# Kernel optimization log

Measured on AMD Instinct MI355X. Metric: run time of the kernel, lower is better.

The kernel has to match this reference:

```python
import jax, jax.numpy as jnp
import numpy as np

N = 8192
E = 262144
D_IN = 256
D_OUT = 256

def setup_inputs() -> dict:
    key = jax.random.key(0)
    k1, k2, k3, k4 = jax.random.split(key, 4)
    x = jax.random.normal(k1, (N, D_IN), dtype=jnp.float32)
    edge_index = jax.random.randint(k2, (2, E), 0, N, dtype=jnp.int64)
    W = jax.random.normal(k3, (D_OUT, D_IN), dtype=jnp.float32) * (1.0 / np.sqrt(D_IN))
    b = jax.random.normal(k4, (D_OUT,), dtype=jnp.float32) * 0.01
    return {"x": x, "edge_index": edge_index, "W": W, "b": b}

def reference(x, edge_index, W, b):
    num_nodes = x.shape[0]
    # dense adjacency: adj[src, dst] = 1.0 (duplicates collapse to 1, matching torch assignment)
    adj = jnp.zeros((num_nodes, num_nodes), dtype=x.dtype)
    adj = adj.at[edge_index[0], edge_index[1]].set(1.0)
    adj = adj + jnp.eye(num_nodes, dtype=x.dtype)  # self-loops (may yield 2.0 if edge had self-loop, as in torch)
    deg = adj.sum(axis=1, keepdims=True)           # [N, 1]
    adj_norm = adj / deg                           # row-normalized
    aggregated = adj_norm @ x                      # [N, D_IN]
    return aggregated @ W.T + b                    # linear: [N, D_OUT]
```

## Files before the change

### kernel.cpp

```cpp
#include <hip/hip_runtime.h>
#include <hip/hip_bf16.h>


#define NNODES 8192
#define DFEAT  256
#define WORDS_PER_ROW (NNODES / 32)

__global__ __launch_bounds__(256) void scatter_edges(
    const int* __restrict__ ei, int E, unsigned* __restrict__ bitmap) {
  int e = blockIdx.x * 256 + threadIdx.x;
  if (e < E) {
    int s = ei[e];
    int d = ei[E + e];
    atomicOr(&bitmap[(size_t)s * WORDS_PER_ROW + (d >> 5)], 1u << (d & 31));
  }
}

#define BM 64
#define BN 64
#define BK 16
__global__ __launch_bounds__(256) void gemm_bias(
    const float* __restrict__ X, const float* __restrict__ W,
    const float* __restrict__ bias, float* __restrict__ Y) {
  __shared__ float As[BK][BM + 4];
  __shared__ float Bs[BK][BN + 4];

  const int bm = blockIdx.x;
  const int bn = blockIdx.y;
  const int tid = threadIdx.x;
  const int tx = tid & 15;
  const int ty = tid >> 4;

  const int lm = tid >> 2;
  const int lk = (tid & 3) * 4;

  const float* Aptr = X + (size_t)(bm * BM + lm) * DFEAT + lk;
  const float* Bptr = W + (size_t)(bn * BN + lm) * DFEAT + lk;

  float c[4][4] = {};

  for (int k0 = 0; k0 < DFEAT; k0 += BK) {
    float4 av = *(const float4*)(Aptr + k0);
    float4 bv = *(const float4*)(Bptr + k0);
    As[lk + 0][lm] = av.x; As[lk + 1][lm] = av.y;
    As[lk + 2][lm] = av.z; As[lk + 3][lm] = av.w;
    Bs[lk + 0][lm] = bv.x; Bs[lk + 1][lm] = bv.y;
    Bs[lk + 2][lm] = bv.z; Bs[lk + 3][lm] = bv.w;
    __syncthreads();
#pragma unroll
    for (int k = 0; k < BK; ++k) {
      float4 a = *(const float4*)&As[k][ty * 4];
      float4 b = *(const float4*)&Bs[k][tx * 4];
      c[0][0] += a.x * b.x; c[0][1] += a.x * b.y; c[0][2] += a.x * b.z; c[0][3] += a.x * b.w;
      c[1][0] += a.y * b.x; c[1][1] += a.y * b.y; c[1][2] += a.y * b.z; c[1][3] += a.y * b.w;
      c[2][0] += a.z * b.x; c[2][1] += a.z * b.y; c[2][2] += a.z * b.z; c[2][3] += a.z * b.w;
      c[3][0] += a.w * b.x; c[3][1] += a.w * b.y; c[3][2] += a.w * b.z; c[3][3] += a.w * b.w;
    }
    __syncthreads();
  }

  const int ocol = bn * BN + tx * 4;
  float4 b4 = *(const float4*)(bias + ocol);
#pragma unroll
  for (int i = 0; i < 4; ++i) {
    const int row = bm * BM + ty * 4 + i;
    float4 r;
    r.x = c[i][0] + b4.x; r.y = c[i][1] + b4.y;
    r.z = c[i][2] + b4.z; r.w = c[i][3] + b4.w;
    *(float4*)(Y + (size_t)row * DFEAT + ocol) = r;
  }
}

__global__ __launch_bounds__(256) void aggregate(
    const unsigned* __restrict__ bitmap, const float* __restrict__ Y,
    float* __restrict__ out) {
  __shared__ unsigned short list[NNODES];
  __shared__ int cnt;

  const int i = blockIdx.x;
  const int tid = threadIdx.x;
  if (tid == 0) cnt = 0;
  __syncthreads();

  unsigned w = bitmap[(size_t)i * WORDS_PER_ROW + tid];
  while (w) {
    int bit = __ffs(w) - 1;
    w &= w - 1;
    int pos = atomicAdd(&cnt, 1);
    list[pos] = (unsigned short)(tid * 32 + bit);
  }
  __syncthreads();

  const int n = cnt;
  float acc0 = 0.f, acc1 = 0.f, acc2 = 0.f, acc3 = 0.f;
  int k = 0;
  for (; k + 4 <= n; k += 4) {
    int j0 = list[k + 0], j1 = list[k + 1], j2 = list[k + 2], j3 = list[k + 3];
    acc0 += Y[(size_t)j0 * DFEAT + tid];
    acc1 += Y[(size_t)j1 * DFEAT + tid];
    acc2 += Y[(size_t)j2 * DFEAT + tid];
    acc3 += Y[(size_t)j3 * DFEAT + tid];
  }
  for (; k < n; ++k) acc0 += Y[(size_t)list[k] * DFEAT + tid];

  float self = Y[(size_t)i * DFEAT + tid];
  float r = (acc0 + acc1 + acc2 + acc3 + self) / (float)(n + 1);
  out[(size_t)i * DFEAT + tid] = r;
}

extern "C" void kernel_launch(void* const* d_in, const int* in_sizes, int n_in,
                              void* d_out, int out_size, void* d_ws, size_t ws_size,
                              hipStream_t stream) {
  const float* x  = (const float*)d_in[0];
  const int*   ei = (const int*)d_in[1];
  const float* W  = (const float*)d_in[2];
  const float* b  = (const float*)d_in[3];
  float* out = (float*)d_out;

  const int E = in_sizes[1] / 2;

  unsigned* bitmap = (unsigned*)d_ws;
  float* Y = (float*)((char*)d_ws + (size_t)NNODES * WORDS_PER_ROW * 4);

  hipMemsetAsync(bitmap, 0, (size_t)NNODES * WORDS_PER_ROW * 4, stream);
  scatter_edges<<<(E + 255) / 256, 256, 0, stream>>>(ei, E, bitmap);
  gemm_bias<<<dim3(NNODES / BM, DFEAT / BN), 256, 0, stream>>>(x, W, b, Y);
  aggregate<<<NNODES, 256, 0, stream>>>(bitmap, Y, out);
}
```

Before: 123.8 us.

## Use split-bf16 MFMA GEMM, build adjacency lists during scatter, split aggregation blocks

```diff
diff --git a/kernel.cpp b/kernel.cpp
--- a/kernel.cpp
+++ b/kernel.cpp
@@ -5,107 +5,126 @@
 #define NNODES 8192
 #define DFEAT  256
 #define WORDS_PER_ROW (NNODES / 32)
+#define MAXDEG 192
 
-__global__ __launch_bounds__(256) void scatter_edges(
-    const int* __restrict__ ei, int E, unsigned* __restrict__ bitmap) {
+typedef __attribute__((ext_vector_type(8))) short   s16x8;
+typedef __attribute__((ext_vector_type(4))) float   f32x4;
+
+__device__ inline unsigned short f2bf(float f) {
+  unsigned u = __float_as_uint(f);
+  return (unsigned short)((u + 0x7fffu + ((u >> 16) & 1u)) >> 16);
+}
+__device__ inline float bf2f(unsigned short h) {
+  return __uint_as_float(((unsigned)h) << 16);
+}
+
+__global__ __launch_bounds__(256) void scatter_build(
+    const int* __restrict__ ei, int E, unsigned* __restrict__ bitmap,
+    int* __restrict__ deg, unsigned short* __restrict__ adj) {
   int e = blockIdx.x * 256 + threadIdx.x;
   if (e < E) {
     int s = ei[e];
     int d = ei[E + e];
-    atomicOr(&bitmap[(size_t)s * WORDS_PER_ROW + (d >> 5)], 1u << (d & 31));
+    unsigned bit = 1u << (d & 31);
+    unsigned old = atomicOr(&bitmap[(size_t)s * WORDS_PER_ROW + (d >> 5)], bit);
+    if (!(old & bit)) {
+      int pos = atomicAdd(&deg[s], 1);
+      if (pos < MAXDEG) adj[(size_t)s * MAXDEG + pos] = (unsigned short)d;
+    }
   }
 }
 
-#define BM 64
-#define BN 64
-#define BK 16
-__global__ __launch_bounds__(256) void gemm_bias(
+__global__ __launch_bounds__(256) void convert_split(
     const float* __restrict__ X, const float* __restrict__ W,
-    const float* __restrict__ bias, float* __restrict__ Y) {
-  __shared__ float As[BK][BM + 4];
-  __shared__ float Bs[BK][BN + 4];
+    unsigned short* __restrict__ Xh, unsigned short* __restrict__ Xl,
+    unsigned short* __restrict__ Wh, unsigned short* __restrict__ Wl) {
+  const int NX = NNODES * DFEAT / 4;
+  const int NW = DFEAT * DFEAT / 4;
+  int i = blockIdx.x * 256 + threadIdx.x;
+  const float* src; unsigned short* dh; unsigned short* dl; int j;
+  if (i < NX)            { src = X; dh = Xh; dl = Xl; j = i; }
+  else if (i < NX + NW)  { src = W; dh = Wh; dl = Wl; j = i - NX; }
+  else return;
+  float4 v = *(const float4*)(src + (size_t)j * 4);
+  ushort4 h, l;
+  h.x = f2bf(v.x); l.x = f2bf(v.x - bf2f(h.x));
+  h.y = f2bf(v.y); l.y = f2bf(v.y - bf2f(h.y));
+  h.z = f2bf(v.z); l.z = f2bf(v.z - bf2f(h.z));
+  h.w = f2bf(v.w); l.w = f2bf(v.w - bf2f(h.w));
+  *(ushort4*)(dh + (size_t)j * 4) = h;
+  *(ushort4*)(dl + (size_t)j * 4) = l;
+}
 
-  const int bm = blockIdx.x;
-  const int bn = blockIdx.y;
-  const int tid = threadIdx.x;
-  const int tx = tid & 15;
-  const int ty = tid >> 4;
+#define GBM 64
+#define GBN 64
+__global__ __launch_bounds__(256) void gemm_mfma(
+    const unsigned short* __restrict__ Xh, const unsigned short* __restrict__ Xl,
+    const unsigned short* __restrict__ Wh, const unsigned short* __restrict__ Wl,
+    float* __restrict__ Y) {
+  const int tid  = threadIdx.x;
+  const int wave = tid >> 6;
+  const int lane = tid & 63;
+  const int row0 = blockIdx.x * GBM + wave * 16;
+  const int col0 = blockIdx.y * GBN;
+  const int lr = lane & 15;
+  const int kh = (lane >> 4) * 8;
 
-  const int lm = tid >> 2;
-  const int lk = (tid & 3) * 4;
+  f32x4 acc[4];
+#pragma unroll
+  for (int i = 0; i < 4; ++i) acc[i] = (f32x4){0.f, 0.f, 0.f, 0.f};
 
-  const float* Aptr = X + (size_t)(bm * BM + lm) * DFEAT + lk;
-  const float* Bptr = W + (size_t)(bn * BN + lm) * DFEAT + lk;
+  const unsigned short* xph = Xh + (size_t)(row0 + lr) * DFEAT + kh;
+  const unsigned short* xpl = Xl + (size_t)(row0 + lr) * DFEAT + kh;
+  const unsigned short* wph = Wh + (size_t)(col0 + lr) * DFEAT + kh;
+  const unsigned short* wpl = Wl + (size_t)(col0 + lr) * DFEAT + kh;
 
-  float c[4][4] = {};
-
-  for (int k0 = 0; k0 < DFEAT; k0 += BK) {
-    float4 av = *(const float4*)(Aptr + k0);
-    float4 bv = *(const float4*)(Bptr + k0);
-    As[lk + 0][lm] = av.x; As[lk + 1][lm] = av.y;
-    As[lk + 2][lm] = av.z; As[lk + 3][lm] = av.w;
-    Bs[lk + 0][lm] = bv.x; Bs[lk + 1][lm] = bv.y;
-    Bs[lk + 2][lm] = bv.z; Bs[lk + 3][lm] = bv.w;
-    __syncthreads();
+  for (int k0 = 0; k0 < DFEAT; k0 += 32) {
+    s16x8 ah = *(const s16x8*)(xph + k0);
+    s16x8 al = *(const s16x8*)(xpl + k0);
 #pragma unroll
-    for (int k = 0; k < BK; ++k) {
-      float4 a = *(const float4*)&As[k][ty * 4];
-      float4 b = *(const float4*)&Bs[k][tx * 4];
-      c[0][0] += a.x * b.x; c[0][1] += a.x * b.y; c[0][2] += a.x * b.z; c[0][3] += a.x * b.w;
-      c[1][0] += a.y * b.x; c[1][1] += a.y * b.y; c[1][2] += a.y * b.z; c[1][3] += a.y * b.w;
-      c[2][0] += a.z * b.x; c[2][1] += a.z * b.y; c[2][2] += a.z * b.z; c[2][3] += a.z * b.w;
-      c[3][0] += a.w * b.x; c[3][1] += a.w * b.y; c[3][2] += a.w * b.z; c[3][3] += a.w * b.w;
+    for (int nt = 0; nt < 4; ++nt) {
+      s16x8 bh = *(const s16x8*)(wph + k0 + nt * 16 * DFEAT);
+      s16x8 bl = *(const s16x8*)(wpl + k0 + nt * 16 * DFEAT);
+      acc[nt] = __builtin_amdgcn_mfma_f32_16x16x32_bf16(ah, bh, acc[nt], 0, 0, 0);
+      acc[nt] = __builtin_amdgcn_mfma_f32_16x16x32_bf16(ah, bl, acc[nt], 0, 0, 0);
+      acc[nt] = __builtin_amdgcn_mfma_f32_16x16x32_bf16(al, bh, acc[nt], 0, 0, 0);
     }
-    __syncthreads();
   }
 
-  const int ocol = bn * BN + tx * 4;
-  float4 b4 = *(const float4*)(bias + ocol);
+  const int crow  = row0 + (lane >> 4) * 4;
+  const int ccol  = col0 + (lane & 15);
 #pragma unroll
-  for (int i = 0; i < 4; ++i) {
-    const int row = bm * BM + ty * 4 + i;
-    float4 r;
-    r.x = c[i][0] + b4.x; r.y = c[i][1] + b4.y;
-    r.z = c[i][2] + b4.z; r.w = c[i][3] + b4.w;
-    *(float4*)(Y + (size_t)row * DFEAT + ocol) = r;
-  }
+  for (int nt = 0; nt < 4; ++nt)
+#pragma unroll
+    for (int r = 0; r < 4; ++r)
+      Y[(size_t)(crow + r) * DFEAT + ccol + nt * 16] = acc[nt][r];
 }
 
-__global__ __launch_bounds__(256) void aggregate(
-    const unsigned* __restrict__ bitmap, const float* __restrict__ Y,
+__global__ __launch_bounds__(64) void aggregate(
+    const int* __restrict__ deg, const unsigned short* __restrict__ adj,
+    const float* __restrict__ Y, const float* __restrict__ bias,
     float* __restrict__ out) {
-  __shared__ unsigned short list[NNODES];
-  __shared__ int cnt;
+  const int b    = blockIdx.x;
+  const int node = b >> 2;
+  const int q    = b & 3;
+  const int ch   = q * 64 + threadIdx.x;
+  const int d    = deg[node];
+  const unsigned short* lst = adj + (size_t)node * MAXDEG;
 
-  const int i = blockIdx.x;
-  const int tid = threadIdx.x;
-  if (tid == 0) cnt = 0;
-  __syncthreads();
+  float a0 = Y[(size_t)node * DFEAT + ch];
+  float a1 = 0.f, a2 = 0.f, a3 = 0.f;
+  int k = 0;
+  for (; k + 4 <= d; k += 4) {
+    int j0 = lst[k], j1 = lst[k + 1], j2 = lst[k + 2], j3 = lst[k + 3];
+    a0 += Y[(size_t)j0 * DFEAT + ch];
+    a1 += Y[(size_t)j1 * DFEAT + ch];
+    a2 += Y[(size_t)j2 * DFEAT + ch];
+    a3 += Y[(size_t)j3 * DFEAT + ch];
+  }
+  for (; k < d; ++k) a0 += Y[(size_t)lst[k] * DFEAT + ch];
 
-  unsigned w = bitmap[(size_t)i * WORDS_PER_ROW + tid];
-  while (w) {
-    int bit = __ffs(w) - 1;
-    w &= w - 1;
-    int pos = atomicAdd(&cnt, 1);
-    list[pos] = (unsigned short)(tid * 32 + bit);
-  }
-  __syncthreads();
-
-  const int n = cnt;
-  float acc0 = 0.f, acc1 = 0.f, acc2 = 0.f, acc3 = 0.f;
-  int k = 0;
-  for (; k + 4 <= n; k += 4) {
-    int j0 = list[k + 0], j1 = list[k + 1], j2 = list[k + 2], j3 = list[k + 3];
-    acc0 += Y[(size_t)j0 * DFEAT + tid];
-    acc1 += Y[(size_t)j1 * DFEAT + tid];
-    acc2 += Y[(size_t)j2 * DFEAT + tid];
-    acc3 += Y[(size_t)j3 * DFEAT + tid];
-  }
-  for (; k < n; ++k) acc0 += Y[(size_t)list[k] * DFEAT + tid];
-
-  float self = Y[(size_t)i * DFEAT + tid];
-  float r = (acc0 + acc1 + acc2 + acc3 + self) / (float)(n + 1);
-  out[(size_t)i * DFEAT + tid] = r;
+  out[(size_t)node * DFEAT + ch] =
+      (a0 + a1 + a2 + a3) / (float)(d + 1) + bias[ch];
 }
 
 extern "C" void kernel_launch(void* const* d_in, const int* in_sizes, int n_in,
@@ -116,14 +135,28 @@
   const float* W  = (const float*)d_in[2];
   const float* b  = (const float*)d_in[3];
   float* out = (float*)d_out;
-
   const int E = in_sizes[1] / 2;
 
-  unsigned* bitmap = (unsigned*)d_ws;
-  float* Y = (float*)((char*)d_ws + (size_t)NNODES * WORDS_PER_ROW * 4);
+  char* p = (char*)d_ws;
+  size_t off = 0;
+  auto take = [&](size_t bytes) { char* r = p + off; off = (off + bytes + 255) & ~(size_t)255; return r; };
+  unsigned*       bitmap = (unsigned*)       take((size_t)NNODES * WORDS_PER_ROW * 4);
+  int*            degp   = (int*)            take((size_t)NNODES * 4);
+  unsigned short* adj    = (unsigned short*) take((size_t)NNODES * MAXDEG * 2);
+  unsigned short* Xh     = (unsigned short*) take((size_t)NNODES * DFEAT * 2);
+  unsigned short* Xl     = (unsigned short*) take((size_t)NNODES * DFEAT * 2);
+  unsigned short* Wh     = (unsigned short*) take((size_t)DFEAT * DFEAT * 2);
+  unsigned short* Wl     = (unsigned short*) take((size_t)DFEAT * DFEAT * 2);
+  float*          Y      = (float*)          take((size_t)NNODES * DFEAT * 4);
 
-  hipMemsetAsync(bitmap, 0, (size_t)NNODES * WORDS_PER_ROW * 4, stream);
-  scatter_edges<<<(E + 255) / 256, 256, 0, stream>>>(ei, E, bitmap);
-  gemm_bias<<<dim3(NNODES / BM, DFEAT / BN), 256, 0, stream>>>(x, W, b, Y);
-  aggregate<<<NNODES, 256, 0, stream>>>(bitmap, Y, out);
+  hipMemsetAsync(bitmap, 0, (size_t)NNODES * WORDS_PER_ROW * 4 + (size_t)NNODES * 4 + 256, stream);
+
+  scatter_build<<<(E + 255) / 256, 256, 0, stream>>>(ei, E, bitmap, degp, adj);
+
+  const int nconv = (NNODES * DFEAT / 4) + (DFEAT * DFEAT / 4);
+  convert_split<<<(nconv + 255) / 256, 256, 0, stream>>>(x, W, Xh, Xl, Wh, Wl);
+
+  gemm_mfma<<<dim3(NNODES / GBM, DFEAT / GBN), 256, 0, stream>>>(Xh, Xl, Wh, Wl, Y);
+
+  aggregate<<<NNODES * 4, 64, 0, stream>>>(degp, adj, Y, b, out);
 }
```

After: 141.5 us. +14.2%, slower.
